# Optimization experiments

Measured on AMD Instinct MI355X. Metric: run time of the kernel, lower is better.

## Reference

```python
import jax, jax.numpy as jnp
import numpy as np

B, S, D = 2, 1024, 1024
NH = 8
QK = 512   # qk_dim = 0.5 * D
V = 1024   # v_dim = 1.0 * D
DQK = QK // NH   # 64
DHV = V // NH    # 128
CAP = 15.0       # gate_soft_cap
NORM_EPS = 1e-6
DENOM_EPS = 1e-6


def soft_cap(x, cap):
    return cap * jnp.tanh(x / cap)


def setup_inputs() -> dict:
    key = jax.random.key(0)
    ks = jax.random.split(key, 8)
    s = 0.02
    return {
        "x": jax.random.normal(ks[0], (B, S, D), jnp.float32),
        "Wq": jax.random.normal(ks[1], (QK, D), jnp.float32) * s,
        "Wk": jax.random.normal(ks[2], (QK, D), jnp.float32) * s,
        "Wv": jax.random.normal(ks[3], (V, D), jnp.float32) * s,
        "Wog": jax.random.normal(ks[4], (V, D), jnp.float32) * s,
        "Wi": jax.random.normal(ks[5], (NH, D), jnp.float32) * s,
        "bi": jnp.zeros((NH,), jnp.float32),
        "Wf": jax.random.normal(ks[6], (NH, D), jnp.float32) * s,
        "bf": jnp.ones((NH,), jnp.float32),  # positive forget bias
        "gamma": jnp.ones((V,), jnp.float32),
        "Wout": jax.random.normal(ks[7], (D, V), jnp.float32) * s,
    }


def _mlstm_recurrent(q, k, v, i_pre, f_pre):
    # q,k: [B,S,NH,DQK]; v: [B,S,NH,DHV]; i_pre,f_pre: [B,S,NH]
    f_log = jax.nn.log_sigmoid(f_pre)
    q_s = q * (DQK ** -0.5)
    # move time to leading axis for scan
    xs = (jnp.moveaxis(q_s, 1, 0), jnp.moveaxis(k, 1, 0), jnp.moveaxis(v, 1, 0),
          jnp.moveaxis(i_pre, 1, 0), jnp.moveaxis(f_log, 1, 0))
    C0 = jnp.zeros((B, NH, DQK, DHV), q.dtype)
    n0 = jnp.zeros((B, NH, DQK), q.dtype)
    m0 = jnp.zeros((B, NH), q.dtype)

    def step(carry, xt):
        C, n, m = carry
        qt, kt, vt, it, ft = xt  # [B,NH,*]
        m_new = jnp.maximum(ft + m, it)                      # [B,NH]
        f_act = jnp.exp(ft + m - m_new)
        i_act = jnp.exp(it - m_new)
        C = f_act[..., None, None] * C + i_act[..., None, None] * (kt[..., :, None] * vt[..., None, :])
        n = f_act[..., None] * n + i_act[..., None] * kt
        h_num = jnp.einsum('bhd,bhdv->bhv', qt, C)
        qn = jnp.einsum('bhd,bhd->bh', qt, n)
        denom = jnp.maximum(jnp.abs(qn), jnp.exp(-m_new)) + DENOM_EPS
        h = h_num / denom[..., None]
        return (C, n, m_new), h

    (C, n, m), hs = jax.lax.scan(step, (C0, n0, m0), xs)
    return jnp.moveaxis(hs, 0, 1), (C, n, m)  # h: [B,S,NH,DHV]


def reference(x, Wq, Wk, Wv, Wog, Wi, bi, Wf, bf, gamma, Wout):
    q = (x @ Wq.T).reshape(B, S, NH, DQK)
    k = (x @ Wk.T).reshape(B, S, NH, DQK)
    v = (x @ Wv.T).reshape(B, S, NH, DHV)
    o_pre = x @ Wog.T                                  # [B,S,V]
    i_pre = soft_cap(x @ Wi.T + bi, CAP)               # [B,S,NH]
    f_pre = soft_cap(x @ Wf.T + bf, CAP)               # [B,S,NH]

    h, _state = _mlstm_recurrent(q, k, v, i_pre, f_pre)  # [B,S,NH,DHV]

    # multi-head layernorm over head dim, float32 reductions
    h32 = h.astype(jnp.float32)
    mu = jnp.mean(h32, axis=-1, keepdims=True)
    var = jnp.mean(jnp.square(h32 - mu), axis=-1, keepdims=True)
    h_norm = ((h32 - mu) * jax.lax.rsqrt(var + NORM_EPS)).astype(h.dtype)
    h_norm = h_norm * gamma.reshape(NH, DHV)
    h_norm = h_norm.reshape(B, S, V)

    h_out = jax.nn.sigmoid(o_pre) * h_norm
    y = h_out @ Wout.T
    return y
```

## Files before the change

### kernel.cpp

```cpp
#include <hip/hip_runtime.h>
#include <hip/hip_bf16.h>
#include <math.h>

typedef __bf16 bf16x8 __attribute__((ext_vector_type(8)));
typedef float f32x4 __attribute__((ext_vector_type(4)));

#define NB 2
#define NS 1024
#define ND 1024
#define NH 8
#define NQK 512
#define NV 1024
#define DQK 64
#define DHV 128
#define CHUNK 64
#define NCHUNK 16

#define GLDS16(g, l) __builtin_amdgcn_global_load_lds((const __attribute__((address_space(1))) void*)(g), (__attribute__((address_space(3))) void*)(l), 16, 0, 0)

static __device__ __forceinline__ void split_bf16(float v, __bf16& hi, __bf16& lo) {
  hi = (__bf16)v;
  lo = (__bf16)(v - (float)hi);
}

static __device__ __forceinline__ int xcd_swz(int orig, int nwg) {
  int q = nwg >> 3, r = nwg & 7;
  int xcd = orig & 7, idx = orig >> 3;
  int base = (xcd < r) ? xcd * (q + 1) : r * (q + 1) + (xcd - r) * q;
  return base + idx;
}

__global__ __launch_bounds__(256) void cvt_all(const float* __restrict__ x,
    const float* __restrict__ wq, const float* __restrict__ wk,
    const float* __restrict__ wv, const float* __restrict__ wog,
    const float* __restrict__ wout,
    __bf16* __restrict__ xb, __bf16* __restrict__ wb, __bf16* __restrict__ wob) {
  long i = (long)blockIdx.x * 256 + threadIdx.x;
  const float* src; __bf16* dst;
  if (i < 524288)        { src = x    + i*4;                    dst = xb  + i*4; }
  else if (i < 655360)   { long j = i -  524288; src = wq  + j*4; dst = wb + j*4; }
  else if (i < 786432)   { long j = i -  655360; src = wk  + j*4; dst = wb +  524288 + j*4; }
  else if (i < 1048576)  { long j = i -  786432; src = wv  + j*4; dst = wb + 1048576 + j*4; }
  else if (i < 1310720)  { long j = i - 1048576; src = wog + j*4; dst = wb + 2097152 + j*4; }
  else                   { long j = i - 1310720; src = wout+ j*4; dst = wob + j*4; }
  float4 v = *(const float4*)src;
  __bf16 o[4];
  o[0] = (__bf16)v.x; o[1] = (__bf16)v.y; o[2] = (__bf16)v.z; o[3] = (__bf16)v.w;
  *(short4*)dst = *(const short4*)o;
}

#define STAGE_AB(Abuf, Bbuf, Aptr, Bptr, Krun, ktv)                           \
  do {                                                                        \
    _Pragma("unroll")                                                         \
    for (int i_ = 0; i_ < 4; ++i_) {                                          \
      const int sb_ = i_ * 256 + wid * 64;                                    \
      const int s_ = sb_ + lane;                                              \
      const int row_ = s_ >> 3;                                               \
      const int klog_ = (s_ & 7) ^ (row_ & 7);                                \
      GLDS16(Aptr + (size_t)(m0 + row_) * Krun + (ktv) * 64 + klog_ * 8, Abuf + sb_ * 8); \
      if (i_ < 2)                                                             \
        GLDS16(Bptr + (size_t)(n0 + row_) * Krun + (ktv) * 64 + klog_ * 8, Bbuf + sb_ * 8); \
    }                                                                         \
  } while (0)

__global__ __launch_bounds__(256) void gemm_bt(const __bf16* __restrict__ A,
                                               const __bf16* __restrict__ Bm,
                                               float* __restrict__ C,
                                               int M, int N, int K, int ntn, int nwg) {
  __shared__ __bf16 smA[2][128 * 64];
  __shared__ __bf16 smB[2][64 * 64];
  const int wg = xcd_swz(blockIdx.x, nwg);
  const int m0 = (wg / ntn) * 128;
  const int n0 = (wg % ntn) * 64;
  const int tid = threadIdx.x;
  const int wid = tid >> 6, lane = tid & 63;
  const int wm = (wid >> 1) * 64, wn = (wid & 1) * 32;
  const int fr = lane & 15;
  const int g  = lane >> 4;
  f32x4 acc[4][2] = {};
  const int NT = K >> 6;
  STAGE_AB(smA[0], smB[0], A, Bm, K, 0);
  int cur = 0;
  for (int kt = 0; kt < NT; ++kt) {
    __syncthreads();
    if (kt + 1 < NT) STAGE_AB(smA[cur ^ 1], smB[cur ^ 1], A, Bm, K, kt + 1);
    #pragma unroll
    for (int kk = 0; kk < 2; ++kk) {
      const int kg = kk * 4 + g;
      bf16x8 af[4], bfv[2];
      #pragma unroll
      for (int f = 0; f < 4; ++f) {
        const int Ra = wm + f * 16 + fr;
        af[f] = *(const bf16x8*)&smA[cur][Ra * 64 + ((kg ^ (Ra & 7)) * 8)];
      }
      #pragma unroll
      for (int n = 0; n < 2; ++n) {
        const int Rb = wn + n * 16 + fr;
        bfv[n] = *(const bf16x8*)&smB[cur][Rb * 64 + ((kg ^ (Rb & 7)) * 8)];
      }
      #pragma unroll
      for (int i = 0; i < 4; ++i)
        #pragma unroll
        for (int j = 0; j < 2; ++j)
          acc[i][j] = __builtin_amdgcn_mfma_f32_16x16x32_bf16(af[i], bfv[j], acc[i][j], 0, 0, 0);
    }
    cur ^= 1;
  }
  const int orow = m0 + wm + g * 4;
  const int ocol = n0 + wn + fr;
  #pragma unroll
  for (int i = 0; i < 4; ++i)
    #pragma unroll
    for (int j = 0; j < 2; ++j)
      #pragma unroll
      for (int r = 0; r < 4; ++r)
        C[(size_t)(orow + i*16 + r) * N + (ocol + j*16)] = acc[i][j][r];
}

__global__ __launch_bounds__(256) void gemm_proj(const __bf16* __restrict__ A,
    const __bf16* __restrict__ Bm,
    __bf16* __restrict__ qh, __bf16* __restrict__ ql,
    __bf16* __restrict__ kh, __bf16* __restrict__ kl,
    __bf16* __restrict__ kT, __bf16* __restrict__ vT,
    _Float16* __restrict__ ogs) {
  __shared__ __bf16 smA[2][128 * 64];
  __shared__ __bf16 smB[2][64 * 64];
  const int wg = xcd_swz(blockIdx.x, 768);
  const int m0 = (wg / 48) * 128;
  const int n0 = (wg % 48) * 64;
  const int tid = threadIdx.x;
  const int wid = tid >> 6, lane = tid & 63;
  const int wm = (wid >> 1) * 64, wn = (wid & 1) * 32;
  const int fr = lane & 15;
  const int g  = lane >> 4;
  f32x4 acc[4][2] = {};
  STAGE_AB(smA[0], smB[0], A, Bm, 1024, 0);
  int cur = 0;
  for (int kt = 0; kt < 16; ++kt) {
    __syncthreads();
    if (kt + 1 < 16) STAGE_AB(smA[cur ^ 1], smB[cur ^ 1], A, Bm, 1024, kt + 1);
    #pragma unroll
    for (int kk = 0; kk < 2; ++kk) {
      const int kg = kk * 4 + g;
      bf16x8 af[4], bfv[2];
      #pragma unroll
      for (int f = 0; f < 4; ++f) {
        const int Ra = wm + f * 16 + fr;
        af[f] = *(const bf16x8*)&smA[cur][Ra * 64 + ((kg ^ (Ra & 7)) * 8)];
      }
      #pragma unroll
      for (int n = 0; n < 2; ++n) {
        const int Rb = wn + n * 16 + fr;
        bfv[n] = *(const bf16x8*)&smB[cur][Rb * 64 + ((kg ^ (Rb & 7)) * 8)];
      }
      #pragma unroll
      for (int i = 0; i < 4; ++i)
        #pragma unroll
        for (int j = 0; j < 2; ++j)
          acc[i][j] = __builtin_amdgcn_mfma_f32_16x16x32_bf16(af[i], bfv[j], acc[i][j], 0, 0, 0);
    }
    cur ^= 1;
  }
  const int orow = m0 + wm + g * 4;
  const int ocol = n0 + wn + fr;
  const int rng = n0 >> 9;
  if (rng == 0 || rng == 1) {
    __bf16* Hb = (rng == 0) ? qh : kh;
    __bf16* Lb = (rng == 0) ? ql : kl;
    const float sc = (rng == 0) ? 0.125f : 1.0f;
    #pragma unroll
    for (int i = 0; i < 4; ++i)
      #pragma unroll
      for (int j = 0; j < 2; ++j) {
        const int col = (ocol + j*16) & 511;
        const int d = col & 63;
        const int hb = col & ~63;
        __bf16 t4[4];
        #pragma unroll
        for (int r = 0; r < 4; ++r) {
          const int row = orow + i*16 + r;
          float v = acc[i][j][r] * sc;
          __bf16 hi, lo; split_bf16(v, hi, lo);
          t4[r] = hi;
          const int off = row*512 + hb + ((((d>>3) ^ (row&7))) << 3) + (d & 7);
          Hb[off] = hi;
          Lb[off] = lo;
        }
        if (rng == 1) {
          const int row0r = orow + i*16;
          const int bh = ((row0r >> 10) << 3) + (col >> 6);
          const int c = (row0r >> 6) & 15;
          const int s0 = (row0r & 63);
          const int off = ((bh*16 + c)*64 + d)*64 + (((s0>>3) ^ (d&7)) << 3) + (s0 & 7);
          *(short4*)&kT[off] = *(const short4*)t4;
        }
      }
  } else if (rng == 2 || rng == 3) {
    #pragma unroll
    for (int i = 0; i < 4; ++i)
      #pragma unroll
      for (int j = 0; j < 2; ++j) {
        const int col = (ocol + j*16) & 1023;
        const int u = col & 127;
        __bf16 t4[4];
        #pragma unroll
        for (int r = 0; r < 4; ++r) t4[r] = (__bf16)acc[i][j][r];
        const int row0r = orow + i*16;
        const int bh = ((row0r >> 10) << 3) + (col >> 7);
        const int c = (row0r >> 6) & 15;
        const int s0 = (row0r & 63);
        const int off = ((bh*16 + c)*128 + u)*64 + (((s0>>3) ^ (u&7)) << 3) + (s0 & 7);
        *(short4*)&vT[off] = *(const short4*)t4;
      }
  } else {
    #pragma unroll
    for (int i = 0; i < 4; ++i)
      #pragma unroll
      for (int j = 0; j < 2; ++j) {
        const int col = (ocol + j*16) & 1023;
        #pragma unroll
        for (int r = 0; r < 4; ++r) {
          const int row = orow + i*16 + r;
          float sg = 1.f / (1.f + __expf(-acc[i][j][r]));
          ogs[(size_t)row*1024 + col] = (_Float16)sg;
        }
      }
  }
}

__global__ __launch_bounds__(256) void ifgate_kernel(const float* __restrict__ x,
    const float* __restrict__ Wi, const float* __restrict__ bi,
    const float* __restrict__ Wf, const float* __restrict__ bf_,
    float* __restrict__ icap, float* __restrict__ flog) {
  const int row = blockIdx.x;
  const int w = threadIdx.x >> 6;
  const int l = threadIdx.x & 63;
  const float* xr = x + (size_t)row * ND;
  float xv[16];
  #pragma unroll
  for (int t = 0; t < 16; ++t) xv[t] = xr[l + 64*t];
  for (int hh = 0; hh < 2; ++hh) {
    int h = w*2 + hh;
    const float* wi = Wi + (size_t)h * ND;
    const float* wf = Wf + (size_t)h * ND;
    float si = 0.f, sf = 0.f;
    #pragma unroll
    for (int t = 0; t < 16; ++t) {
      si += xv[t] * wi[l + 64*t];
      sf += xv[t] * wf[l + 64*t];
    }
    #pragma unroll
    for (int off = 32; off; off >>= 1) {
      si += __shfl_xor(si, off, 64);
      sf += __shfl_xor(sf, off, 64);
    }
    if (l == 0) {
      float ic = 15.f * tanhf((si + bi[h]) * (1.f/15.f));
      float fc = 15.f * tanhf((sf + bf_[h]) * (1.f/15.f));
      float fl = (fc >= 0.f) ? -log1pf(__expf(-fc)) : (fc - log1pf(__expf(fc)));
      icap[row*NH + h] = ic;
      flog[row*NH + h] = fl;
    }
  }
}

__global__ __launch_bounds__(64) void gates_kernel(const float* __restrict__ icap,
    const float* __restrict__ flog, float* __restrict__ g_g, float* __restrict__ a_g,
    float* __restrict__ m_g, float* __restrict__ m0g) {
  const int bh = blockIdx.x;
  const int b = bh >> 3, h = bh & 7;
  const int l = threadIdx.x;
  float m0 = 0.f;
  for (int c = 0; c < NCHUNK; ++c) {
    const int t = c*CHUNK + l;
    const int row = b*NS + t;
    float B = flog[row*NH + h];
    float iv = icap[row*NH + h];
    #pragma unroll
    for (int d = 1; d < 64; d <<= 1) {
      float o = __shfl_up(B, d, 64);
      if (l >= d) B += o;
    }
    float g = iv - B;
    float cm = g;
    #pragma unroll
    for (int d = 1; d < 64; d <<= 1) {
      float o = __shfl_up(cm, d, 64);
      if (l >= d) cm = fmaxf(cm, o);
    }
    float a = fmaxf(m0, cm);
    float m = B + a;
    const int idx = bh*NS + t;
    g_g[idx] = g; a_g[idx] = a; m_g[idx] = m;
    if (l == 0) m0g[bh*NCHUNK + c] = m0;
    m0 = __shfl(m, 63, 64);
  }
}

__global__ __launch_bounds__(256) void u_kernel(const __bf16* __restrict__ kT,
    const __bf16* __restrict__ vT, const float* __restrict__ g_g,
    const float* __restrict__ a_g, float* __restrict__ Ut, float* __restrict__ Ung) {
  __shared__ __bf16 kts[64 * 64];
  __shared__ __bf16 vts[128 * 64];
  __shared__ float w_l[64];
  const int task = blockIdx.x;
  const int bh = task >> 4, c = task & 15;
  const int t = threadIdx.x;
  const int wid = t >> 6, lane = t & 63;
  const int fr = lane & 15, g = lane >> 4;
  if (t < 64) {
    const float aL = a_g[bh*NS + c*CHUNK + 63];
    w_l[t] = __expf(g_g[bh*NS + c*CHUNK + t] - aL);
  }
  {
    const int sb = wid * 64;
    #pragma unroll
    for (int i = 0; i < 2; ++i) {
      const int s = i*256 + sb + lane;
      GLDS16(kT + (size_t)task*4096 + s*8, kts + (i*256 + sb)*8);
    }
    #pragma unroll
    for (int i = 0; i < 4; ++i) {
      const int s = i*256 + sb + lane;
      GLDS16(vT + (size_t)task*8192 + s*8, vts + (i*256 + sb)*8);
    }
  }
  __syncthreads();
  f32x4 acc[8] = {};
  #pragma unroll
  for (int kk = 0; kk < 2; ++kk) {
    const int kg = kk*4 + g;
    const int Ra = wid*16 + fr;
    bf16x8 afr = *(const bf16x8*)&kts[Ra*64 + ((kg ^ (Ra & 7)) * 8)];
    bf16x8 afw;
    #pragma unroll
    for (int j = 0; j < 8; ++j) afw[j] = (__bf16)((float)afr[j] * w_l[kg*8 + j]);
    #pragma unroll
    for (int nt = 0; nt < 8; ++nt) {
      const int Rb = nt*16 + fr;
      bf16x8 bv = *(const bf16x8*)&vts[Rb*64 + ((kg ^ (Rb & 7)) * 8)];
      acc[nt] = __builtin_amdgcn_mfma_f32_16x16x32_bf16(afw, bv, acc[nt], 0, 0, 0);
    }
  }
  float* ub = Ut + (size_t)task * 8192;
  #pragma unroll
  for (int nt = 0; nt < 8; ++nt) {
    const int u = nt*16 + fr;
    *(f32x4*)&ub[u*64 + wid*16 + g*4] = acc[nt];
  }
  if (t < 64) {
    float s = 0.f;
    #pragma unroll
    for (int blk = 0; blk < 8; ++blk) {
      bf16x8 kv = *(const bf16x8*)&kts[t*64 + ((blk ^ (t & 7)) * 8)];
      #pragma unroll
      for (int j = 0; j < 8; ++j) s += (float)kv[j] * w_l[blk*8 + j];
    }
    Ung[task*64 + t] = s;
  }
}

__global__ __launch_bounds__(64) void statescan_kernel(const float* __restrict__ Ut,
    const float* __restrict__ Ung, const float* __restrict__ m0g,
    const float* __restrict__ a_g, __bf16* __restrict__ C0T, float* __restrict__ n0g) {
  const int bh = blockIdx.x >> 4, part = blockIdx.x & 15;
  const int e8 = part*64 + threadIdx.x;
  const int u = e8 >> 3, d8 = e8 & 7;
  const int dsto = u*64 + ((d8 ^ (u & 7)) << 3);
  const int srco = u*64 + d8*8;
  float scale[NCHUNK];
  #pragma unroll
  for (int c = 0; c < NCHUNK; ++c)
    scale[c] = __expf(m0g[bh*NCHUNK + c] - a_g[bh*NS + c*CHUNK + 63]);
  float val[8] = {};
  for (int c = 0; c < NCHUNK; ++c) {
    const size_t base = ((size_t)(bh*NCHUNK + c)) * 8192;
    __bf16 o[8];
    #pragma unroll
    for (int j = 0; j < 8; ++j) o[j] = (__bf16)val[j];
    *(float4*)&C0T[base + dsto] = *(const float4*)o;
    f32x4 u0 = *(const f32x4*)&Ut[base + srco];
    f32x4 u1 = *(const f32x4*)&Ut[base + srco + 4];
    #pragma unroll
    for (int j = 0; j < 4; ++j) {
      val[j]   = scale[c]*val[j]   + u0[j];
      val[j+4] = scale[c]*val[j+4] + u1[j];
    }
  }
  if (part == 0) {
    float nv = 0.f;
    for (int c = 0; c < NCHUNK; ++c) {
      int idx = (bh*NCHUNK + c)*64 + threadIdx.x;
      n0g[idx] = nv;
      nv = scale[c]*nv + Ung[idx];
    }
  }
}

__global__ __launch_bounds__(256) void intra_kernel(
    const __bf16* __restrict__ qh, const __bf16* __restrict__ ql,
    const __bf16* __restrict__ kh, const __bf16* __restrict__ kl,
    const __bf16* __restrict__ vT, const __bf16* __restrict__ C0T,
    const _Float16* __restrict__ ogs,
    const float* __restrict__ g_g, const float* __restrict__ a_g,
    const float* __restrict__ m_g, const float* __restrict__ m0g,
    const float* __restrict__ n0g,
    const float* __restrict__ gamma, __bf16* __restrict__ hout) {
  __shared__ __bf16 qh_s[32*64], ql_s[32*64];
  __shared__ __bf16 kh_s[64*64], kl_s[64*64];
  __shared__ __bf16 vt_s[128*64];
  __shared__ __bf16 c0_s[128*64];
  __shared__ __bf16 Ps[32*72];
  __shared__ float g_l[64], n0_l[64], a_l[32], m_l[32], cI_l[32];
  __shared__ float qnA[2][32], qnI_l[32], lnS[2][32], lnQ[2][32];

  const int blk = blockIdx.x;
  const int task = blk >> 1, jhalf = blk & 1;
  const int bh = task >> 4, c = task & 15;
  const int b = bh >> 3, h = bh & 7;
  const int t = threadIdx.x;
  const int wid = t >> 6, lane = t & 63;
  const int fr = lane & 15, lg = lane >> 4;
  const int jt_local = wid >> 1, half = wid & 1;
  const int jtg = jhalf*2 + jt_local;
  const int row0 = b*NS + c*CHUNK;
  const int jrow0 = row0 + jhalf*32;

  {
    const int sb = wid * 64;
    {
      const int s = sb + lane;
      const int r = s >> 3, bk = s & 7;
      const size_t go = (size_t)(jrow0 + r)*512 + h*64 + bk*8;
      GLDS16(qh + go, qh_s + sb*8);
      GLDS16(ql + go, ql_s + sb*8);
    }
    #pragma unroll
    for (int i = 0; i < 2; ++i) {
      const int s = i*256 + sb + lane;
      const int r = s >> 3, bk = s & 7;
      const size_t go = (size_t)(row0 + r)*512 + h*64 + bk*8;
      GLDS16(kh + go, kh_s + (i*256 + sb)*8);
      GLDS16(kl + go, kl_s + (i*256 + sb)*8);
    }
    #pragma unroll
    for (int i = 0; i < 4; ++i) {
      const int s = i*256 + sb + lane;
      GLDS16(vT  + (size_t)task*8192 + s*8, vt_s + (i*256 + sb)*8);
      GLDS16(C0T + (size_t)task*8192 + s*8, c0_s + (i*256 + sb)*8);
    }
  }
  const float m0v = m0g[bh*NCHUNK + c];
  if (t < 64) {
    g_l[t]  = g_g[bh*NS + c*CHUNK + t];
    n0_l[t] = n0g[task*64 + t];
  } else if (t < 96) {
    int jl = t - 64;
    float av = a_g[bh*NS + c*CHUNK + jhalf*32 + jl];
    a_l[jl] = av;
    m_l[jl] = m_g[bh*NS + c*CHUNK + jhalf*32 + jl];
    cI_l[jl] = __expf(m0v - av);
  }
  __syncthreads();

  float rsum[4] = {0.f, 0.f, 0.f, 0.f};
  for (int st = half; st < 4; st += 2) {
    if (st <= jtg) {
      f32x4 sacc = {};
      #pragma unroll
      for (int kk = 0; kk < 2; ++kk) {
        const int kg = kk*4 + lg;
        const int Ra = jt_local*16 + fr;
        const int Rb = st*16 + fr;
        bf16x8 qhv = *(const bf16x8*)&qh_s[Ra*64 + ((kg ^ (Ra&7))*8)];
        bf16x8 qlv = *(const bf16x8*)&ql_s[Ra*64 + ((kg ^ (Ra&7))*8)];
        bf16x8 khv = *(const bf16x8*)&kh_s[Rb*64 + ((kg ^ (Rb&7))*8)];
        bf16x8 klv = *(const bf16x8*)&kl_s[Rb*64 + ((kg ^ (Rb&7))*8)];
        sacc = __builtin_amdgcn_mfma_f32_16x16x32_bf16(qhv, khv, sacc, 0, 0, 0);
        sacc = __builtin_amdgcn_mfma_f32_16x16x32_bf16(qhv, klv, sacc, 0, 0, 0);
        sacc = __builtin_amdgcn_mfma_f32_16x16x32_bf16(qlv, khv, sacc, 0, 0, 0);
      }
      const int s_c = st*16 + fr;
      const float gs = g_l[s_c];
      #pragma unroll
      for (int r = 0; r < 4; ++r) {
        const int jl = jt_local*16 + lg*4 + r;
        const int j_c = jhalf*32 + jl;
        float w = (s_c <= j_c) ? __expf(gs - a_l[jl]) : 0.f;
        float p = sacc[r] * w;
        rsum[r] += p;
        Ps[jl*72 + s_c] = (__bf16)p;
      }
    } else {
      #pragma unroll
      for (int r = 0; r < 4; ++r)
        Ps[(jt_local*16 + lg*4 + r)*72 + st*16 + fr] = (__bf16)0.f;
    }
  }
  #pragma unroll
  for (int r = 0; r < 4; ++r) {
    #pragma unroll
    for (int off = 1; off < 16; off <<= 1) rsum[r] += __shfl_xor(rsum[r], off, 64);
  }
  if (fr == 0) {
    #pragma unroll
    for (int r = 0; r < 4; ++r) qnA[half][jt_local*16 + lg*4 + r] = rsum[r];
  }

  f32x4 acc[4] = {};
  #pragma unroll
  for (int kk = 0; kk < 2; ++kk) {
    const int kg = kk*4 + lg;
    const int Ra = jt_local*16 + fr;
    bf16x8 aq = *(const bf16x8*)&qh_s[Ra*64 + ((kg ^ (Ra&7))*8)];
    #pragma unroll
    for (int nt = 0; nt < 4; ++nt) {
      const int Rb = (half*4 + nt)*16 + fr;
      bf16x8 bc = *(const bf16x8*)&c0_s[Rb*64 + ((kg ^ (Rb&7))*8)];
      acc[nt] = __builtin_amdgcn_mfma_f32_16x16x32_bf16(aq, bc, acc[nt], 0, 0, 0);
    }
  }
  {
    float ci4[4];
    #pragma unroll
    for (int r = 0; r < 4; ++r) ci4[r] = cI_l[jt_local*16 + lg*4 + r];
    #pragma unroll
    for (int nt = 0; nt < 4; ++nt)
      #pragma unroll
      for (int r = 0; r < 4; ++r) acc[nt][r] *= ci4[r];
  }
  if (half == 1) {
    const int jl = jt_local*16 + fr;
    float s = 0.f;
    #pragma unroll
    for (int i = 0; i < 16; ++i) {
      const int d = lg*16 + i;
      const int off = jl*64 + (((d>>3) ^ (jl&7)) << 3) + (d & 7);
      float qv = (float)qh_s[off] + (float)ql_s[off];
      s += qv * n0_l[d];
    }
    s += __shfl_xor(s, 16, 64);
    s += __shfl_xor(s, 32, 64);
    if (lane < 16) qnI_l[jl] = cI_l[jl] * s;
  }
  __syncthreads();

  #pragma unroll
  for (int kk = 0; kk < 2; ++kk) {
    const int kg = kk*4 + lg;
    bf16x8 ap = *(const bf16x8*)&Ps[(jt_local*16 + fr)*72 + kg*8];
    #pragma unroll
    for (int nt = 0; nt < 4; ++nt) {
      const int Rb = (half*4 + nt)*16 + fr;
      bf16x8 bv = *(const bf16x8*)&vt_s[Rb*64 + ((kg ^ (Rb&7))*8)];
      acc[nt] = __builtin_amdgcn_mfma_f32_16x16x32_bf16(ap, bv, acc[nt], 0, 0, 0);
    }
  }

  #pragma unroll
  for (int r = 0; r < 4; ++r) {
    const int jl = jt_local*16 + lg*4 + r;
    float qn = qnA[0][jl] + qnA[1][jl] + qnI_l[jl];
    float denom = fmaxf(fabsf(qn), __expf(-m_l[jl])) + 1e-6f;
    float rd = 1.f / denom;
    float s = 0.f, q2 = 0.f;
    #pragma unroll
    for (int nt = 0; nt < 4; ++nt) {
      float hv = acc[nt][r] * rd;
      acc[nt][r] = hv;
      s += hv; q2 += hv*hv;
    }
    #pragma unroll
    for (int off = 1; off < 16; off <<= 1) {
      s  += __shfl_xor(s,  off, 64);
      q2 += __shfl_xor(q2, off, 64);
    }
    if (fr == 0) { lnS[half][jl] = s; lnQ[half][jl] = q2; }
  }
  __syncthreads();

  #pragma unroll
  for (int r = 0; r < 4; ++r) {
    const int jl = jt_local*16 + lg*4 + r;
    float sm = lnS[0][jl] + lnS[1][jl];
    float sq = lnQ[0][jl] + lnQ[1][jl];
    float mu = sm * (1.f/128.f);
    float var = sq * (1.f/128.f) - mu*mu;
    float rstd = rsqrtf(var + 1e-6f);
    const int rowg = jrow0 + jl;
    #pragma unroll
    for (int nt = 0; nt < 4; ++nt) {
      const int u = (half*4 + nt)*16 + fr;
      float sg = (float)ogs[(size_t)rowg*1024 + h*DHV + u];
      float hn = (acc[nt][r] - mu) * rstd * gamma[h*DHV + u] * sg;
      hout[(size_t)rowg*NV + h*DHV + u] = (__bf16)hn;
    }
  }
}

extern "C" void kernel_launch(void* const* d_in, const int* in_sizes, int n_in,
                              void* d_out, int out_size, void* d_ws, size_t ws_size,
                              hipStream_t stream) {
  const float* x    = (const float*)d_in[0];
  const float* Wq   = (const float*)d_in[1];
  const float* Wk   = (const float*)d_in[2];
  const float* Wv   = (const float*)d_in[3];
  const float* Wog  = (const float*)d_in[4];
  const float* Wi   = (const float*)d_in[5];
  const float* bi   = (const float*)d_in[6];
  const float* Wf   = (const float*)d_in[7];
  const float* bf_  = (const float*)d_in[8];
  const float* gamma= (const float*)d_in[9];
  const float* Wout = (const float*)d_in[10];
  float* y = (float*)d_out;

  char* ws = (char*)d_ws;
  const size_t MB = 1u << 20;
  __bf16*   xb   = (__bf16*)  (ws + 0);
  __bf16*   Wb   = (__bf16*)  (ws + 4*MB);
  __bf16*   Wob  = (__bf16*)  (ws + 10*MB);
  __bf16*   qh   = (__bf16*)  (ws + 12*MB);
  __bf16*   ql   = (__bf16*)  (ws + 14*MB);
  __bf16*   kh   = (__bf16*)  (ws + 16*MB);
  __bf16*   kl   = (__bf16*)  (ws + 18*MB);
  __bf16*   kT   = (__bf16*)  (ws + 20*MB);
  __bf16*   vT   = (__bf16*)  (ws + 22*MB);
  _Float16* ogs  = (_Float16*)(ws + 26*MB);
  float*    Ut   = (float*)   (ws + 30*MB);
  __bf16*   C0T  = (__bf16*)  (ws + 38*MB);
  float*    icap = (float*)   (ws + 42*MB);
  float*    flog = (float*)   (ws + 42*MB + 64*1024);
  float*    g_g  = (float*)   (ws + 42*MB + 128*1024);
  float*    a_g  = (float*)   (ws + 42*MB + 192*1024);
  float*    m_g  = (float*)   (ws + 42*MB + 256*1024);
  float*    m0g  = (float*)   (ws + 42*MB + 320*1024);
  float*    Ung  = (float*)   (ws + 42*MB + 384*1024);
  float*    n0g  = (float*)   (ws + 42*MB + 448*1024);
  __bf16*   houtb= (__bf16*)  (ws + 44*MB);

  cvt_all<<<6144, 256, 0, stream>>>(x, Wq, Wk, Wv, Wog, Wout, xb, Wb, Wob);

  gemm_proj<<<768, 256, 0, stream>>>(xb, Wb, qh, ql, kh, kl, kT, vT, ogs);

  ifgate_kernel<<<2048, 256, 0, stream>>>(x, Wi, bi, Wf, bf_, icap, flog);
  gates_kernel<<<16, 64, 0, stream>>>(icap, flog, g_g, a_g, m_g, m0g);
  u_kernel<<<256, 256, 0, stream>>>(kT, vT, g_g, a_g, Ut, Ung);
  statescan_kernel<<<256, 64, 0, stream>>>(Ut, Ung, m0g, a_g, C0T, n0g);
  intra_kernel<<<512, 256, 0, stream>>>(qh, ql, kh, kl, vT, C0T, ogs,
                                        g_g, a_g, m_g, m0g, n0g, gamma, houtb);

  gemm_bt<<<256, 256, 0, stream>>>(houtb, Wob, y, 2048, 1024, 1024, 16, 256);
}
```

Before: 171.4 us.

## Fuse gate projection into prep kernel and read operands directly from global

Merges the input/forget gate projection into the bf16 conversion kernel as extra blocks, which removes one kernel launch and lets both parts run concurrently. Separately, u_kernel and intra_kernel drop their LDS staging of k, v, q and C0 tiles and load MFMA operands straight from global memory into registers. The q fragments are also hoisted into registers and reused. This cuts LDS traffic and the shared-memory footprint, which may raise occupancy. The trade-off is repeated, less coalesced global loads that depend on L1/L2 hits.

```diff
diff --git a/kernel.cpp b/kernel.cpp
--- a/kernel.cpp
+++ b/kernel.cpp
@@ -30,23 +30,59 @@
   return base + idx;
 }
 
-__global__ __launch_bounds__(256) void cvt_all(const float* __restrict__ x,
+__global__ __launch_bounds__(256) void prep_kernel(const float* __restrict__ x,
     const float* __restrict__ wq, const float* __restrict__ wk,
     const float* __restrict__ wv, const float* __restrict__ wog,
     const float* __restrict__ wout,
-    __bf16* __restrict__ xb, __bf16* __restrict__ wb, __bf16* __restrict__ wob) {
-  long i = (long)blockIdx.x * 256 + threadIdx.x;
-  const float* src; __bf16* dst;
-  if (i < 524288)        { src = x    + i*4;                    dst = xb  + i*4; }
-  else if (i < 655360)   { long j = i -  524288; src = wq  + j*4; dst = wb + j*4; }
-  else if (i < 786432)   { long j = i -  655360; src = wk  + j*4; dst = wb +  524288 + j*4; }
-  else if (i < 1048576)  { long j = i -  786432; src = wv  + j*4; dst = wb + 1048576 + j*4; }
-  else if (i < 1310720)  { long j = i - 1048576; src = wog + j*4; dst = wb + 2097152 + j*4; }
-  else                   { long j = i - 1310720; src = wout+ j*4; dst = wob + j*4; }
-  float4 v = *(const float4*)src;
-  __bf16 o[4];
-  o[0] = (__bf16)v.x; o[1] = (__bf16)v.y; o[2] = (__bf16)v.z; o[3] = (__bf16)v.w;
-  *(short4*)dst = *(const short4*)o;
+    const float* __restrict__ Wi, const float* __restrict__ bi,
+    const float* __restrict__ Wf, const float* __restrict__ bf_,
+    __bf16* __restrict__ xb, __bf16* __restrict__ wb, __bf16* __restrict__ wob,
+    float* __restrict__ icap, float* __restrict__ flog) {
+  if (blockIdx.x < 6144) {
+    long i = (long)blockIdx.x * 256 + threadIdx.x;
+    const float* src; __bf16* dst;
+    if (i < 524288)        { src = x    + i*4;                    dst = xb  + i*4; }
+    else if (i < 655360)   { long j = i -  524288; src = wq  + j*4; dst = wb + j*4; }
+    else if (i < 786432)   { long j = i -  655360; src = wk  + j*4; dst = wb +  524288 + j*4; }
+    else if (i < 1048576)  { long j = i -  786432; src = wv  + j*4; dst = wb + 1048576 + j*4; }
+    else if (i < 1310720)  { long j = i - 1048576; src = wog + j*4; dst = wb + 2097152 + j*4; }
+    else                   { long j = i - 1310720; src = wout+ j*4; dst = wob + j*4; }
+    float4 v = *(const float4*)src;
+    __bf16 o[4];
+    o[0] = (__bf16)v.x; o[1] = (__bf16)v.y; o[2] = (__bf16)v.z; o[3] = (__bf16)v.w;
+    *(short4*)dst = *(const short4*)o;
+  } else {
+    const int row = blockIdx.x - 6144;
+    const int w = threadIdx.x >> 6;
+    const int l = threadIdx.x & 63;
+    const float* xr = x + (size_t)row * ND;
+    float xv[16];
+    #pragma unroll
+    for (int t = 0; t < 16; ++t) xv[t] = xr[l + 64*t];
+    for (int hh = 0; hh < 2; ++hh) {
+      int h = w*2 + hh;
+      const float* wi = Wi + (size_t)h * ND;
+      const float* wf = Wf + (size_t)h * ND;
+      float si = 0.f, sf = 0.f;
+      #pragma unroll
+      for (int t = 0; t < 16; ++t) {
+        si += xv[t] * wi[l + 64*t];
+        sf += xv[t] * wf[l + 64*t];
+      }
+      #pragma unroll
+      for (int off = 32; off; off >>= 1) {
+        si += __shfl_xor(si, off, 64);
+        sf += __shfl_xor(sf, off, 64);
+      }
+      if (l == 0) {
+        float ic = 15.f * tanhf((si + bi[h]) * (1.f/15.f));
+        float fc = 15.f * tanhf((sf + bf_[h]) * (1.f/15.f));
+        float fl = (fc >= 0.f) ? -log1pf(__expf(-fc)) : (fc - log1pf(__expf(fc)));
+        icap[row*NH + h] = ic;
+        flog[row*NH + h] = fl;
+      }
+    }
+  }
 }
 
 #define STAGE_AB(Abuf, Bbuf, Aptr, Bptr, Krun, ktv)                           \
@@ -228,42 +264,6 @@
   }
 }
 
-__global__ __launch_bounds__(256) void ifgate_kernel(const float* __restrict__ x,
-    const float* __restrict__ Wi, const float* __restrict__ bi,
-    const float* __restrict__ Wf, const float* __restrict__ bf_,
-    float* __restrict__ icap, float* __restrict__ flog) {
-  const int row = blockIdx.x;
-  const int w = threadIdx.x >> 6;
-  const int l = threadIdx.x & 63;
-  const float* xr = x + (size_t)row * ND;
-  float xv[16];
-  #pragma unroll
-  for (int t = 0; t < 16; ++t) xv[t] = xr[l + 64*t];
-  for (int hh = 0; hh < 2; ++hh) {
-    int h = w*2 + hh;
-    const float* wi = Wi + (size_t)h * ND;
-    const float* wf = Wf + (size_t)h * ND;
-    float si = 0.f, sf = 0.f;
-    #pragma unroll
-    for (int t = 0; t < 16; ++t) {
-      si += xv[t] * wi[l + 64*t];
-      sf += xv[t] * wf[l + 64*t];
-    }
-    #pragma unroll
-    for (int off = 32; off; off >>= 1) {
-      si += __shfl_xor(si, off, 64);
-      sf += __shfl_xor(sf, off, 64);
-    }
-    if (l == 0) {
-      float ic = 15.f * tanhf((si + bi[h]) * (1.f/15.f));
-      float fc = 15.f * tanhf((sf + bf_[h]) * (1.f/15.f));
-      float fl = (fc >= 0.f) ? -log1pf(__expf(-fc)) : (fc - log1pf(__expf(fc)));
-      icap[row*NH + h] = ic;
-      flog[row*NH + h] = fl;
-    }
-  }
-}
-
 __global__ __launch_bounds__(64) void gates_kernel(const float* __restrict__ icap,
     const float* __restrict__ flog, float* __restrict__ g_g, float* __restrict__ a_g,
     float* __restrict__ m_g, float* __restrict__ m0g) {
@@ -300,8 +300,6 @@
 __global__ __launch_bounds__(256) void u_kernel(const __bf16* __restrict__ kT,
     const __bf16* __restrict__ vT, const float* __restrict__ g_g,
     const float* __restrict__ a_g, float* __restrict__ Ut, float* __restrict__ Ung) {
-  __shared__ __bf16 kts[64 * 64];
-  __shared__ __bf16 vts[128 * 64];
   __shared__ float w_l[64];
   const int task = blockIdx.x;
   const int bh = task >> 4, c = task & 15;
@@ -312,33 +310,22 @@
     const float aL = a_g[bh*NS + c*CHUNK + 63];
     w_l[t] = __expf(g_g[bh*NS + c*CHUNK + t] - aL);
   }
-  {
-    const int sb = wid * 64;
-    #pragma unroll
-    for (int i = 0; i < 2; ++i) {
-      const int s = i*256 + sb + lane;
-      GLDS16(kT + (size_t)task*4096 + s*8, kts + (i*256 + sb)*8);
-    }
-    #pragma unroll
-    for (int i = 0; i < 4; ++i) {
-      const int s = i*256 + sb + lane;
-      GLDS16(vT + (size_t)task*8192 + s*8, vts + (i*256 + sb)*8);
-    }
-  }
   __syncthreads();
+  const __bf16* ktb = kT + (size_t)task * 4096;
+  const __bf16* vtb = vT + (size_t)task * 8192;
   f32x4 acc[8] = {};
   #pragma unroll
   for (int kk = 0; kk < 2; ++kk) {
     const int kg = kk*4 + g;
     const int Ra = wid*16 + fr;
-    bf16x8 afr = *(const bf16x8*)&kts[Ra*64 + ((kg ^ (Ra & 7)) * 8)];
+    bf16x8 afr = *(const bf16x8*)&ktb[Ra*64 + ((kg ^ (Ra & 7)) * 8)];
     bf16x8 afw;
     #pragma unroll
     for (int j = 0; j < 8; ++j) afw[j] = (__bf16)((float)afr[j] * w_l[kg*8 + j]);
     #pragma unroll
     for (int nt = 0; nt < 8; ++nt) {
       const int Rb = nt*16 + fr;
-      bf16x8 bv = *(const bf16x8*)&vts[Rb*64 + ((kg ^ (Rb & 7)) * 8)];
+      bf16x8 bv = *(const bf16x8*)&vtb[Rb*64 + ((kg ^ (Rb & 7)) * 8)];
       acc[nt] = __builtin_amdgcn_mfma_f32_16x16x32_bf16(afw, bv, acc[nt], 0, 0, 0);
     }
   }
@@ -352,7 +339,7 @@
     float s = 0.f;
     #pragma unroll
     for (int blk = 0; blk < 8; ++blk) {
-      bf16x8 kv = *(const bf16x8*)&kts[t*64 + ((blk ^ (t & 7)) * 8)];
+      bf16x8 kv = *(const bf16x8*)&ktb[t*64 + ((blk ^ (t & 7)) * 8)];
       #pragma unroll
       for (int j = 0; j < 8; ++j) s += (float)kv[j] * w_l[blk*8 + j];
     }
@@ -406,10 +393,6 @@
     const float* __restrict__ m_g, const float* __restrict__ m0g,
     const float* __restrict__ n0g,
     const float* __restrict__ gamma, __bf16* __restrict__ hout) {
-  __shared__ __bf16 qh_s[32*64], ql_s[32*64];
-  __shared__ __bf16 kh_s[64*64], kl_s[64*64];
-  __shared__ __bf16 vt_s[128*64];
-  __shared__ __bf16 c0_s[128*64];
   __shared__ __bf16 Ps[32*72];
   __shared__ float g_l[64], n0_l[64], a_l[32], m_l[32], cI_l[32];
   __shared__ float qnA[2][32], qnI_l[32], lnS[2][32], lnQ[2][32];
@@ -425,31 +408,9 @@
   const int jtg = jhalf*2 + jt_local;
   const int row0 = b*NS + c*CHUNK;
   const int jrow0 = row0 + jhalf*32;
-
-  {
-    const int sb = wid * 64;
-    {
-      const int s = sb + lane;
-      const int r = s >> 3, bk = s & 7;
-      const size_t go = (size_t)(jrow0 + r)*512 + h*64 + bk*8;
-      GLDS16(qh + go, qh_s + sb*8);
-      GLDS16(ql + go, ql_s + sb*8);
-    }
-    #pragma unroll
-    for (int i = 0; i < 2; ++i) {
-      const int s = i*256 + sb + lane;
-      const int r = s >> 3, bk = s & 7;
-      const size_t go = (size_t)(row0 + r)*512 + h*64 + bk*8;
-      GLDS16(kh + go, kh_s + (i*256 + sb)*8);
-      GLDS16(kl + go, kl_s + (i*256 + sb)*8);
-    }
-    #pragma unroll
-    for (int i = 0; i < 4; ++i) {
-      const int s = i*256 + sb + lane;
-      GLDS16(vT  + (size_t)task*8192 + s*8, vt_s + (i*256 + sb)*8);
-      GLDS16(C0T + (size_t)task*8192 + s*8, c0_s + (i*256 + sb)*8);
-    }
-  }
+  const __bf16* vtb = vT + (size_t)task * 8192;
+  const __bf16* c0b = C0T + (size_t)task * 8192;
+
   const float m0v = m0g[bh*NCHUNK + c];
   if (t < 64) {
     g_l[t]  = g_g[bh*NS + c*CHUNK + t];
@@ -463,22 +424,32 @@
   }
   __syncthreads();
 
+  const int Ra = jt_local*16 + fr;
+  const size_t qrow = (size_t)(jrow0 + Ra)*512 + h*64;
+  bf16x8 qhv[2], qlv[2];
+  #pragma unroll
+  for (int kk = 0; kk < 2; ++kk) {
+    const int kg = kk*4 + lg;
+    const int off = (kg ^ (Ra & 7)) * 8;
+    qhv[kk] = *(const bf16x8*)&qh[qrow + off];
+    qlv[kk] = *(const bf16x8*)&ql[qrow + off];
+  }
+
   float rsum[4] = {0.f, 0.f, 0.f, 0.f};
   for (int st = half; st < 4; st += 2) {
     if (st <= jtg) {
       f32x4 sacc = {};
+      const int Rb = st*16 + fr;
+      const size_t krow = (size_t)(row0 + Rb)*512 + h*64;
       #pragma unroll
       for (int kk = 0; kk < 2; ++kk) {
         const int kg = kk*4 + lg;
-        const int Ra = jt_local*16 + fr;
-        const int Rb = st*16 + fr;
-        bf16x8 qhv = *(const bf16x8*)&qh_s[Ra*64 + ((kg ^ (Ra&7))*8)];
-        bf16x8 qlv = *(const bf16x8*)&ql_s[Ra*64 + ((kg ^ (Ra&7))*8)];
-        bf16x8 khv = *(const bf16x8*)&kh_s[Rb*64 + ((kg ^ (Rb&7))*8)];
-        bf16x8 klv = *(const bf16x8*)&kl_s[Rb*64 + ((kg ^ (Rb&7))*8)];
-        sacc = __builtin_amdgcn_mfma_f32_16x16x32_bf16(qhv, khv, sacc, 0, 0, 0);
-        sacc = __builtin_amdgcn_mfma_f32_16x16x32_bf16(qhv, klv, sacc, 0, 0, 0);
-        sacc = __builtin_amdgcn_mfma_f32_16x16x32_bf16(qlv, khv, sacc, 0, 0, 0);
+        const int offb = (kg ^ (Rb & 7)) * 8;
+        bf16x8 khv = *(const bf16x8*)&kh[krow + offb];
+        bf16x8 klv = *(const bf16x8*)&kl[krow + offb];
+        sacc = __builtin_amdgcn_mfma_f32_16x16x32_bf16(qhv[kk], khv, sacc, 0, 0, 0);
+        sacc = __builtin_amdgcn_mfma_f32_16x16x32_bf16(qhv[kk], klv, sacc, 0, 0, 0);
+        sacc = __builtin_amdgcn_mfma_f32_16x16x32_bf16(qlv[kk], khv, sacc, 0, 0, 0);
       }
       const int s_c = st*16 + fr;
       const float gs = g_l[s_c];
@@ -511,13 +482,11 @@
   #pragma unroll
   for (int kk = 0; kk < 2; ++kk) {
     const int kg = kk*4 + lg;
-    const int Ra = jt_local*16 + fr;
-    bf16x8 aq = *(const bf16x8*)&qh_s[Ra*64 + ((kg ^ (Ra&7))*8)];
     #pragma unroll
     for (int nt = 0; nt < 4; ++nt) {
       const int Rb = (half*4 + nt)*16 + fr;
-      bf16x8 bc = *(const bf16x8*)&c0_s[Rb*64 + ((kg ^ (Rb&7))*8)];
-      acc[nt] = __builtin_amdgcn_mfma_f32_16x16x32_bf16(aq, bc, acc[nt], 0, 0, 0);
+      bf16x8 bc = *(const bf16x8*)&c0b[Rb*64 + ((kg ^ (Rb&7))*8)];
+      acc[nt] = __builtin_amdgcn_mfma_f32_16x16x32_bf16(qhv[kk], bc, acc[nt], 0, 0, 0);
     }
   }
   {
@@ -531,12 +500,13 @@
   }
   if (half == 1) {
     const int jl = jt_local*16 + fr;
+    const size_t qr2 = (size_t)(jrow0 + jl)*512 + h*64;
     float s = 0.f;
     #pragma unroll
     for (int i = 0; i < 16; ++i) {
       const int d = lg*16 + i;
-      const int off = jl*64 + (((d>>3) ^ (jl&7)) << 3) + (d & 7);
-      float qv = (float)qh_s[off] + (float)ql_s[off];
+      const int off = (((d>>3) ^ (jl&7)) << 3) + (d & 7);
+      float qv = (float)qh[qr2 + off] + (float)ql[qr2 + off];
       s += qv * n0_l[d];
     }
     s += __shfl_xor(s, 16, 64);
@@ -552,7 +522,7 @@
     #pragma unroll
     for (int nt = 0; nt < 4; ++nt) {
       const int Rb = (half*4 + nt)*16 + fr;
-      bf16x8 bv = *(const bf16x8*)&vt_s[Rb*64 + ((kg ^ (Rb&7))*8)];
+      bf16x8 bv = *(const bf16x8*)&vtb[Rb*64 + ((kg ^ (Rb&7))*8)];
       acc[nt] = __builtin_amdgcn_mfma_f32_16x16x32_bf16(ap, bv, acc[nt], 0, 0, 0);
     }
   }
@@ -638,11 +608,11 @@
   float*    n0g  = (float*)   (ws + 42*MB + 448*1024);
   __bf16*   houtb= (__bf16*)  (ws + 44*MB);
 
-  cvt_all<<<6144, 256, 0, stream>>>(x, Wq, Wk, Wv, Wog, Wout, xb, Wb, Wob);
+  prep_kernel<<<8192, 256, 0, stream>>>(x, Wq, Wk, Wv, Wog, Wout, Wi, bi, Wf, bf_,
+                                        xb, Wb, Wob, icap, flog);
 
   gemm_proj<<<768, 256, 0, stream>>>(xb, Wb, qh, ql, kh, kl, kT, vT, ogs);
 
-  ifgate_kernel<<<2048, 256, 0, stream>>>(x, Wi, bi, Wf, bf_, icap, flog);
   gates_kernel<<<16, 64, 0, stream>>>(icap, flog, g_g, a_g, m_g, m0g);
   u_kernel<<<256, 256, 0, stream>>>(kT, vT, g_g, a_g, Ut, Ung);
   statescan_kernel<<<256, 64, 0, stream>>>(Ut, Ung, m0g, a_g, C0T, n0g);
```

Result: faster. 163.4 us (-4.7%).
